# Performance work log

Hardware: AMD Instinct MI355X
Metric: run time of the kernel (lower is better)

The kernel has to match this reference:

```python
import jax, jax.numpy as jnp
import numpy as np

N = 100000
E = 1600000
IN_DIM = 128
HID = 64
NCOMM = 32


def setup_inputs() -> dict:
    key = jax.random.key(0)
    k = jax.random.split(key, 8)
    x = jax.random.normal(k[0], (N, IN_DIM), dtype=jnp.float32)
    edge_index = jax.random.randint(k[1], (2, E), 0, N, dtype=jnp.int64)
    s1 = 1.0 / np.sqrt(IN_DIM)
    s2 = 1.0 / np.sqrt(HID)
    W1 = jax.random.uniform(k[2], (IN_DIM, HID), jnp.float32, -s1, s1)
    b1 = jnp.zeros((HID,), jnp.float32)
    W2 = jax.random.uniform(k[3], (HID, HID), jnp.float32, -s2, s2)
    b2 = jnp.zeros((HID,), jnp.float32)
    Wfc = jax.random.uniform(k[4], (HID, NCOMM), jnp.float32, -s2, s2)
    bfc = jax.random.uniform(k[5], (NCOMM,), jnp.float32, -s2, s2)
    return {"x": x, "edge_index": edge_index, "W1": W1, "b1": b1,
            "W2": W2, "b2": b2, "Wfc": Wfc, "bfc": bfc}


def gcn_conv(x, row, col, norm, W, b):
    # PyG GCNConv: linear -> gather(source) * norm -> scatter_add(target) -> + bias
    h = x @ W                                    # [N, out]
    msgs = h[row] * norm[:, None]                # [E+N, out] gather (memory-bound)
    agg = jax.ops.segment_sum(msgs, col, num_segments=x.shape[0])
    return agg + b


def reference(x, edge_index, W1, b1, W2, b2, Wfc, bfc):
    n = x.shape[0]
    # add self-loops (PyG GCNConv default)
    loop = jnp.arange(n, dtype=edge_index.dtype)
    row = jnp.concatenate([edge_index[0], loop])  # source
    col = jnp.concatenate([edge_index[1], loop])  # target
    # symmetric normalization D^{-1/2} (A+I) D^{-1/2}
    deg = jax.ops.segment_sum(jnp.ones_like(col, dtype=x.dtype), col, num_segments=n)
    dinv = jnp.where(deg > 0, jax.lax.rsqrt(deg), 0.0)
    norm = dinv[row] * dinv[col]
    h = jax.nn.relu(gcn_conv(x, row, col, norm, W1, b1))   # dropout = identity (eval)
    h = jax.nn.relu(gcn_conv(h, row, col, norm, W2, b2))
    return jax.nn.sigmoid(h @ Wfc + bfc)
```

## Files before the change

kernel.cpp:

```cpp
#include <hip/hip_runtime.h>
#include <hip/hip_fp16.h>
#include <math.h>

#define N_NODES 100000
#define N_EDGES 1600000
#define IN_DIM  128
#define HID     64
#define NCOMM   32
#define NB        391
#define BSHIFT    8
#define EPB       4096
#define NBIN_BLK  391

typedef _Float16 f16x8 __attribute__((ext_vector_type(8)));
typedef float    f32x4 __attribute__((ext_vector_type(4)));

__global__ void k_detect(const unsigned int* __restrict__ e, int* __restrict__ flag) {
  int lane = threadIdx.x;
  unsigned v = 0;
  #pragma unroll
  for (int i = 0; i < 4; ++i) v |= e[2 * (lane * 4 + i) + 1];
  unsigned long long nz = __ballot(v != 0u);
  if (lane == 0) *flag = (nz == 0ull) ? 1 : 0;
}

__device__ __forceinline__ int load_idx(const int* e32, long long pos, int is64) {
  if (is64) return (int)(((const long long*)e32)[pos]);
  return e32[pos];
}

__global__ __launch_bounds__(256) void k_bhist(const int* __restrict__ e, int* __restrict__ bcnt,
                                               const int* __restrict__ flag) {
  __shared__ int cnt[NB];
  for (int i = threadIdx.x; i < NB; i += 256) cnt[i] = 0;
  __syncthreads();
  int is64 = *flag;
  long long base = (long long)blockIdx.x * EPB;
  #pragma unroll
  for (int j = 0; j < EPB / 256; ++j) {
    long long eid = base + j * 256 + threadIdx.x;
    if (eid < N_EDGES) {
      int c = load_idx(e, (long long)N_EDGES + eid, is64);
      atomicAdd(&cnt[c >> BSHIFT], 1);
    }
  }
  __syncthreads();
  for (int b = threadIdx.x; b < NB; b += 256)
    if (cnt[b]) atomicAdd(&bcnt[b], cnt[b]);
}

__global__ __launch_bounds__(512) void k_bscan(const int* __restrict__ bcnt, int* __restrict__ bptr,
                                               int* __restrict__ bcur) {
  __shared__ int sm[512];
  int t = threadIdx.x;
  int v = (t < NB) ? bcnt[t] : 0;
  sm[t] = v;
  __syncthreads();
  for (int off = 1; off < 512; off <<= 1) {
    int u = (t >= off) ? sm[t - off] : 0;
    __syncthreads();
    sm[t] += u;
    __syncthreads();
  }
  if (t < NB) {
    int ex = sm[t] - v;
    bptr[t] = ex;
    bcur[t] = ex;
  }
  if (t == 0) bptr[NB] = N_EDGES;
}

__global__ __launch_bounds__(256) void k_bin(const int* __restrict__ e, int* __restrict__ bcur,
                                             unsigned* __restrict__ ebuf, const int* __restrict__ flag) {
  __shared__ int cnt[NB];
  __shared__ int base[NB];
  for (int i = threadIdx.x; i < NB; i += 256) cnt[i] = 0;
  __syncthreads();
  int is64 = *flag;
  long long eb = (long long)blockIdx.x * EPB;
  int rr[EPB / 256], cc[EPB / 256], lr[EPB / 256];
  #pragma unroll
  for (int j = 0; j < EPB / 256; ++j) {
    long long eid = eb + j * 256 + threadIdx.x;
    if (eid < N_EDGES) {
      rr[j] = load_idx(e, eid, is64);
      cc[j] = load_idx(e, (long long)N_EDGES + eid, is64);
      lr[j] = atomicAdd(&cnt[cc[j] >> BSHIFT], 1);
    }
  }
  __syncthreads();
  for (int b = threadIdx.x; b < NB; b += 256)
    base[b] = cnt[b] ? atomicAdd(&bcur[b], cnt[b]) : 0;
  __syncthreads();
  #pragma unroll
  for (int j = 0; j < EPB / 256; ++j) {
    long long eid = eb + j * 256 + threadIdx.x;
    if (eid < N_EDGES) {
      int pos = base[cc[j] >> BSHIFT] + lr[j];
      ebuf[pos] = ((unsigned)(cc[j] & 255) << 17) | (unsigned)rr[j];
    }
  }
}

__global__ __launch_bounds__(256) void k_degsort(const unsigned* __restrict__ ebuf, const int* __restrict__ bptr,
                                                 float* __restrict__ dinv, int* __restrict__ ptr,
                                                 int* __restrict__ srow) {
  __shared__ int cnt[256];
  __shared__ int scn[256];
  __shared__ int cur[256];
  int t = threadIdx.x;
  int b = blockIdx.x;
  int c0 = b << BSHIFT;
  cnt[t] = 0;
  __syncthreads();
  int s = bptr[b], epos = bptr[b + 1];
  for (int i = s + t; i < epos; i += 256)
    atomicAdd(&cnt[ebuf[i] >> 17], 1);
  __syncthreads();
  int d = cnt[t];
  scn[t] = d;
  __syncthreads();
  for (int off = 1; off < 256; off <<= 1) {
    int u = (t >= off) ? scn[t - off] : 0;
    __syncthreads();
    scn[t] += u;
    __syncthreads();
  }
  int myptr = s + scn[t] - d;
  int node = c0 + t;
  if (node < N_NODES) {
    dinv[node] = rsqrtf((float)d + 1.0f);
    ptr[node] = myptr;
  }
  cur[t] = myptr;
  __syncthreads();
  for (int i = s + t; i < epos; i += 256) {
    unsigned w = ebuf[i];
    int pos = atomicAdd(&cur[w >> 17], 1);
    srow[pos] = (int)(w & 0x1FFFFu);
  }
  if (b == NB - 1 && t == 0) ptr[N_NODES] = N_EDGES;
}

template<int K, int M, bool FINAL, bool INH>
__global__ __launch_bounds__(256) void k_mfma(const void* __restrict__ X, const float* __restrict__ W,
                                              void* __restrict__ Y, const float* __restrict__ bias,
                                              const float* __restrict__ dscale) {
  constexpr int NN = M / 16;
  constexpr int KS = K / 32;
  __shared__ char smem[M * K * 2];

  const int tid = threadIdx.x;
  for (int i = tid; i < K * M / 4; i += 256) {
    int k  = i / (M / 4);
    int mf = (i % (M / 4)) * 4;
    float4 wv = *(const float4*)(W + (size_t)k * M + mf);
    float wa[4] = {wv.x, wv.y, wv.z, wv.w};
    #pragma unroll
    for (int c = 0; c < 4; ++c) {
      int m = mf + c;
      int byte_off = m * (2 * K) + ((((k >> 3) << 4)) ^ ((m & 7) << 4)) + (k & 7) * 2;
      *(_Float16*)(smem + byte_off) = (_Float16)wa[c];
    }
  }
  __syncthreads();

  const int lane = tid & 63;
  const int wv_  = tid >> 6;
  const int rowbase = blockIdx.x * 128 + wv_ * 32;
  const int lr = lane & 15;
  const int kg = lane >> 4;
  const int r0 = rowbase + lr;
  const int r1 = r0 + 16;
  const int rc0 = (r0 < N_NODES) ? r0 : (N_NODES - 1);
  const int rc1 = (r1 < N_NODES) ? r1 : (N_NODES - 1);

  f32x4 acc[2][NN] = {};

  #pragma unroll
  for (int ks = 0; ks < KS; ++ks) {
    const int k0 = ks * 32 + kg * 8;
    f16x8 a0, a1;
    if constexpr (!INH) {
      const float* xr = (const float*)X;
      float4 u0 = *(const float4*)(xr + (size_t)rc0 * K + k0);
      float4 u1 = *(const float4*)(xr + (size_t)rc0 * K + k0 + 4);
      float4 u2 = *(const float4*)(xr + (size_t)rc1 * K + k0);
      float4 u3 = *(const float4*)(xr + (size_t)rc1 * K + k0 + 4);
      a0[0] = (_Float16)u0.x; a0[1] = (_Float16)u0.y; a0[2] = (_Float16)u0.z; a0[3] = (_Float16)u0.w;
      a0[4] = (_Float16)u1.x; a0[5] = (_Float16)u1.y; a0[6] = (_Float16)u1.z; a0[7] = (_Float16)u1.w;
      a1[0] = (_Float16)u2.x; a1[1] = (_Float16)u2.y; a1[2] = (_Float16)u2.z; a1[3] = (_Float16)u2.w;
      a1[4] = (_Float16)u3.x; a1[5] = (_Float16)u3.y; a1[6] = (_Float16)u3.z; a1[7] = (_Float16)u3.w;
    } else {
      const char* xb = (const char*)X;
      a0 = *(const f16x8*)(xb + (size_t)rc0 * (2 * K) + k0 * 2);
      a1 = *(const f16x8*)(xb + (size_t)rc1 * (2 * K) + k0 * 2);
    }
    const int slot = (k0 >> 3) << 4;
    #pragma unroll
    for (int n = 0; n < NN; ++n) {
      const int col = n * 16 + lr;
      f16x8 b = *(const f16x8*)(smem + col * (2 * K) + (slot ^ ((col & 7) << 4)));
      acc[0][n] = __builtin_amdgcn_mfma_f32_16x16x32_f16(a0, b, acc[0][n], 0, 0, 0);
      acc[1][n] = __builtin_amdgcn_mfma_f32_16x16x32_f16(a1, b, acc[1][n], 0, 0, 0);
    }
  }

  #pragma unroll
  for (int m2 = 0; m2 < 2; ++m2) {
    #pragma unroll
    for (int r = 0; r < 4; ++r) {
      const int row = rowbase + m2 * 16 + kg * 4 + r;
      if (row < N_NODES) {
        float ds = FINAL ? 0.f : dscale[row];
        #pragma unroll
        for (int n = 0; n < NN; ++n) {
          const int col = n * 16 + lr;
          float v = acc[m2][n][r];
          if constexpr (FINAL) {
            v += bias[col];
            v = 1.f / (1.f + __expf(-v));
            ((float*)Y)[(size_t)row * M + col] = v;
          } else {
            ((__half*)Y)[(size_t)row * M + col] = __float2half(v * ds);
          }
        }
      }
    }
  }
}

__device__ __forceinline__ void addrow(float* acc, uint4 h) {
  __half2 p0 = *(__half2*)&h.x;
  __half2 p1 = *(__half2*)&h.y;
  __half2 p2 = *(__half2*)&h.z;
  __half2 p3 = *(__half2*)&h.w;
  float2 f0 = __half22float2(p0);
  float2 f1 = __half22float2(p1);
  float2 f2 = __half22float2(p2);
  float2 f3 = __half22float2(p3);
  acc[0] += f0.x; acc[1] += f0.y;
  acc[2] += f1.x; acc[3] += f1.y;
  acc[4] += f2.x; acc[5] += f2.y;
  acc[6] += f3.x; acc[7] += f3.y;
}

__global__ __launch_bounds__(256) void k_agg(const __half* __restrict__ H, __half* __restrict__ O,
                                             const int* __restrict__ ptr, const int* __restrict__ srow,
                                             const float* __restrict__ dinv, const float* __restrict__ bias) {
  int wid  = (blockIdx.x * 256 + threadIdx.x) >> 6;
  int lane = threadIdx.x & 63;
  if (wid >= N_NODES) return;
  const int q  = lane >> 3;
  const int fl = lane & 7;
  const char* Hb = (const char*)H;
  int s = ptr[wid], e = ptr[wid + 1];
  float acc[8] = {0.f, 0.f, 0.f, 0.f, 0.f, 0.f, 0.f, 0.f};
  for (int j = s; j < e; j += 16) {
    int i0 = j + q;
    int i1 = j + 8 + q;
    int r0 = srow[i0];
    int r1 = srow[i1];
    r0 = (i0 < e) ? r0 : N_NODES;
    r1 = (i1 < e) ? r1 : N_NODES;
    uint4 h0 = *(const uint4*)(Hb + (size_t)((unsigned)r0 * 128u + (unsigned)fl * 16u));
    uint4 h1 = *(const uint4*)(Hb + (size_t)((unsigned)r1 * 128u + (unsigned)fl * 16u));
    addrow(acc, h0);
    addrow(acc, h1);
  }
  if (q == 0) {
    uint4 hb = *(const uint4*)(Hb + (size_t)((unsigned)wid * 128u + (unsigned)fl * 16u));
    addrow(acc, hb);
  }
  #pragma unroll
  for (int m = 8; m < 64; m <<= 1) {
    #pragma unroll
    for (int i = 0; i < 8; ++i) acc[i] += __shfl_xor(acc[i], m, 64);
  }
  if (lane < 8) {
    float di = dinv[wid];
    float4 ba = ((const float4*)bias)[2 * fl + 0];
    float4 bb = ((const float4*)bias)[2 * fl + 1];
    __half2 o0 = __floats2half2_rn(fmaxf(acc[0] * di + ba.x, 0.f), fmaxf(acc[1] * di + ba.y, 0.f));
    __half2 o1 = __floats2half2_rn(fmaxf(acc[2] * di + ba.z, 0.f), fmaxf(acc[3] * di + ba.w, 0.f));
    __half2 o2 = __floats2half2_rn(fmaxf(acc[4] * di + bb.x, 0.f), fmaxf(acc[5] * di + bb.y, 0.f));
    __half2 o3 = __floats2half2_rn(fmaxf(acc[6] * di + bb.z, 0.f), fmaxf(acc[7] * di + bb.w, 0.f));
    uint4 pv;
    pv.x = *(unsigned*)&o0;
    pv.y = *(unsigned*)&o1;
    pv.z = *(unsigned*)&o2;
    pv.w = *(unsigned*)&o3;
    *(uint4*)((char*)O + (size_t)wid * (HID * 2) + fl * 16) = pv;
  }
}

extern "C" void kernel_launch(void* const* d_in, const int* in_sizes, int n_in,
                              void* d_out, int out_size, void* d_ws, size_t ws_size,
                              hipStream_t stream) {
  const float* x   = (const float*)d_in[0];
  const int*   e   = (const int*)d_in[1];
  const float* W1  = (const float*)d_in[2];
  const float* b1  = (const float*)d_in[3];
  const float* W2  = (const float*)d_in[4];
  const float* b2  = (const float*)d_in[5];
  const float* Wfc = (const float*)d_in[6];
  const float* bfc = (const float*)d_in[7];
  float* out = (float*)d_out;

  char* ws = (char*)d_ws;
  __half*   hbuf = (__half*)  (ws);
  unsigned* ebuf = (unsigned*)(ws);
  int*      srow = (int*)     (ws + 12800256);
  __half*   abuf = (__half*)  (ws + 19200320);
  float*    dinv = (float*)   (ws + 32000320);
  int*      ptr  = (int*)     (ws + 32400320);
  int*      flag = (int*)     (ws + 32800384);
  int*      bcnt = (int*)     (ws + 32800448);
  int*      bptr = (int*)     (ws + 32802048);
  int*      bcur = (int*)     (ws + 32803712);

  hipMemsetAsync(bcnt, 0, NB * sizeof(int), stream);
  hipMemsetAsync(ws + (size_t)N_NODES * 128, 0, 128, stream);
  k_detect<<<1, 64, 0, stream>>>((const unsigned int*)e, flag);
  k_bhist<<<NBIN_BLK, 256, 0, stream>>>(e, bcnt, flag);
  k_bscan<<<1, 512, 0, stream>>>(bcnt, bptr, bcur);
  k_bin<<<NBIN_BLK, 256, 0, stream>>>(e, bcur, ebuf, flag);
  k_degsort<<<NB, 256, 0, stream>>>(ebuf, bptr, dinv, ptr, srow);

  const int gBlocks = (N_NODES + 127) / 128;
  k_mfma<IN_DIM, HID, false, false><<<gBlocks, 256, 0, stream>>>(x, W1, hbuf, nullptr, dinv);
  k_agg<<<N_NODES * 64 / 256, 256, 0, stream>>>(hbuf, abuf, ptr, srow, dinv, b1);
  k_mfma<HID, HID, false, true><<<gBlocks, 256, 0, stream>>>(abuf, W2, hbuf, nullptr, dinv);
  k_agg<<<N_NODES * 64 / 256, 256, 0, stream>>>(hbuf, abuf, ptr, srow, dinv, b2);
  k_mfma<HID, NCOMM, true, true><<<gBlocks, 256, 0, stream>>>(abuf, Wfc, out, bfc, nullptr);
}
```

Baseline: 203.8 us.

## Use fixed-capacity bins to drop histogram/scan passes and reshape aggregation

New measurement: 219.8 us. +7.9%, slower.

```diff
diff --git a/kernel.cpp b/kernel.cpp
--- a/kernel.cpp
+++ b/kernel.cpp
@@ -9,6 +9,7 @@
 #define NCOMM   32
 #define NB        391
 #define BSHIFT    8
+#define BCAP      6144
 #define EPB       4096
 #define NBIN_BLK  391
 
@@ -29,48 +30,7 @@
   return e32[pos];
 }
 
-__global__ __launch_bounds__(256) void k_bhist(const int* __restrict__ e, int* __restrict__ bcnt,
-                                               const int* __restrict__ flag) {
-  __shared__ int cnt[NB];
-  for (int i = threadIdx.x; i < NB; i += 256) cnt[i] = 0;
-  __syncthreads();
-  int is64 = *flag;
-  long long base = (long long)blockIdx.x * EPB;
-  #pragma unroll
-  for (int j = 0; j < EPB / 256; ++j) {
-    long long eid = base + j * 256 + threadIdx.x;
-    if (eid < N_EDGES) {
-      int c = load_idx(e, (long long)N_EDGES + eid, is64);
-      atomicAdd(&cnt[c >> BSHIFT], 1);
-    }
-  }
-  __syncthreads();
-  for (int b = threadIdx.x; b < NB; b += 256)
-    if (cnt[b]) atomicAdd(&bcnt[b], cnt[b]);
-}
-
-__global__ __launch_bounds__(512) void k_bscan(const int* __restrict__ bcnt, int* __restrict__ bptr,
-                                               int* __restrict__ bcur) {
-  __shared__ int sm[512];
-  int t = threadIdx.x;
-  int v = (t < NB) ? bcnt[t] : 0;
-  sm[t] = v;
-  __syncthreads();
-  for (int off = 1; off < 512; off <<= 1) {
-    int u = (t >= off) ? sm[t - off] : 0;
-    __syncthreads();
-    sm[t] += u;
-    __syncthreads();
-  }
-  if (t < NB) {
-    int ex = sm[t] - v;
-    bptr[t] = ex;
-    bcur[t] = ex;
-  }
-  if (t == 0) bptr[NB] = N_EDGES;
-}
-
-__global__ __launch_bounds__(256) void k_bin(const int* __restrict__ e, int* __restrict__ bcur,
+__global__ __launch_bounds__(256) void k_bin(const int* __restrict__ e, int* __restrict__ bcnt,
                                              unsigned* __restrict__ ebuf, const int* __restrict__ flag) {
   __shared__ int cnt[NB];
   __shared__ int base[NB];
@@ -90,32 +50,37 @@
   }
   __syncthreads();
   for (int b = threadIdx.x; b < NB; b += 256)
-    base[b] = cnt[b] ? atomicAdd(&bcur[b], cnt[b]) : 0;
+    base[b] = cnt[b] ? atomicAdd(&bcnt[b], cnt[b]) : 0;
   __syncthreads();
   #pragma unroll
   for (int j = 0; j < EPB / 256; ++j) {
     long long eid = eb + j * 256 + threadIdx.x;
     if (eid < N_EDGES) {
-      int pos = base[cc[j] >> BSHIFT] + lr[j];
+      int bb = cc[j] >> BSHIFT;
+      int pos = bb * BCAP + base[bb] + lr[j];
       ebuf[pos] = ((unsigned)(cc[j] & 255) << 17) | (unsigned)rr[j];
     }
   }
 }
 
-__global__ __launch_bounds__(256) void k_degsort(const unsigned* __restrict__ ebuf, const int* __restrict__ bptr,
-                                                 float* __restrict__ dinv, int* __restrict__ ptr,
+__global__ __launch_bounds__(256) void k_degsort(const unsigned* __restrict__ ebuf, const int* __restrict__ bcnt,
+                                                 float* __restrict__ dinv, int2* __restrict__ parr,
                                                  int* __restrict__ srow) {
   __shared__ int cnt[256];
   __shared__ int scn[256];
   __shared__ int cur[256];
+  __shared__ unsigned eds[BCAP];
   int t = threadIdx.x;
   int b = blockIdx.x;
   int c0 = b << BSHIFT;
+  int n = bcnt[b];
   cnt[t] = 0;
   __syncthreads();
-  int s = bptr[b], epos = bptr[b + 1];
-  for (int i = s + t; i < epos; i += 256)
-    atomicAdd(&cnt[ebuf[i] >> 17], 1);
+  for (int i = t; i < n; i += 256) {
+    unsigned w = ebuf[b * BCAP + i];
+    eds[i] = w;
+    atomicAdd(&cnt[w >> 17], 1);
+  }
   __syncthreads();
   int d = cnt[t];
   scn[t] = d;
@@ -126,20 +91,19 @@
     scn[t] += u;
     __syncthreads();
   }
-  int myptr = s + scn[t] - d;
+  int sabs = b * BCAP + scn[t] - d;
   int node = c0 + t;
   if (node < N_NODES) {
     dinv[node] = rsqrtf((float)d + 1.0f);
-    ptr[node] = myptr;
-  }
-  cur[t] = myptr;
-  __syncthreads();
-  for (int i = s + t; i < epos; i += 256) {
-    unsigned w = ebuf[i];
+    parr[node] = make_int2(sabs, sabs + d);
+  }
+  cur[t] = sabs;
+  __syncthreads();
+  for (int i = t; i < n; i += 256) {
+    unsigned w = eds[i];
     int pos = atomicAdd(&cur[w >> 17], 1);
     srow[pos] = (int)(w & 0x1FFFFu);
   }
-  if (b == NB - 1 && t == 0) ptr[N_NODES] = N_EDGES;
 }
 
 template<int K, int M, bool FINAL, bool INH>
@@ -230,67 +194,36 @@
   }
 }
 
-__device__ __forceinline__ void addrow(float* acc, uint4 h) {
-  __half2 p0 = *(__half2*)&h.x;
-  __half2 p1 = *(__half2*)&h.y;
-  __half2 p2 = *(__half2*)&h.z;
-  __half2 p3 = *(__half2*)&h.w;
-  float2 f0 = __half22float2(p0);
-  float2 f1 = __half22float2(p1);
-  float2 f2 = __half22float2(p2);
-  float2 f3 = __half22float2(p3);
-  acc[0] += f0.x; acc[1] += f0.y;
-  acc[2] += f1.x; acc[3] += f1.y;
-  acc[4] += f2.x; acc[5] += f2.y;
-  acc[6] += f3.x; acc[7] += f3.y;
-}
-
 __global__ __launch_bounds__(256) void k_agg(const __half* __restrict__ H, __half* __restrict__ O,
-                                             const int* __restrict__ ptr, const int* __restrict__ srow,
+                                             const int2* __restrict__ parr, const int* __restrict__ srow,
                                              const float* __restrict__ dinv, const float* __restrict__ bias) {
   int wid  = (blockIdx.x * 256 + threadIdx.x) >> 6;
   int lane = threadIdx.x & 63;
   if (wid >= N_NODES) return;
-  const int q  = lane >> 3;
-  const int fl = lane & 7;
+  const int hf = lane >> 5;
+  const int fl = lane & 31;
   const char* Hb = (const char*)H;
-  int s = ptr[wid], e = ptr[wid + 1];
-  float acc[8] = {0.f, 0.f, 0.f, 0.f, 0.f, 0.f, 0.f, 0.f};
-  for (int j = s; j < e; j += 16) {
-    int i0 = j + q;
-    int i1 = j + 8 + q;
-    int r0 = srow[i0];
-    int r1 = srow[i1];
-    r0 = (i0 < e) ? r0 : N_NODES;
-    r1 = (i1 < e) ? r1 : N_NODES;
-    uint4 h0 = *(const uint4*)(Hb + (size_t)((unsigned)r0 * 128u + (unsigned)fl * 16u));
-    uint4 h1 = *(const uint4*)(Hb + (size_t)((unsigned)r1 * 128u + (unsigned)fl * 16u));
-    addrow(acc, h0);
-    addrow(acc, h1);
-  }
-  if (q == 0) {
-    uint4 hb = *(const uint4*)(Hb + (size_t)((unsigned)wid * 128u + (unsigned)fl * 16u));
-    addrow(acc, hb);
-  }
-  #pragma unroll
-  for (int m = 8; m < 64; m <<= 1) {
-    #pragma unroll
-    for (int i = 0; i < 8; ++i) acc[i] += __shfl_xor(acc[i], m, 64);
-  }
-  if (lane < 8) {
+  int2 se = parr[wid];
+  float ax = 0.f, ay = 0.f;
+  #pragma unroll 2
+  for (int j = se.x + hf; j < se.y; j += 2) {
+    int r = srow[j];
+    unsigned h = *(const unsigned*)(Hb + (size_t)r * 128 + fl * 4);
+    float2 f = __half22float2(*(__half2*)&h);
+    ax += f.x; ay += f.y;
+  }
+  if (hf == 0) {
+    unsigned h = *(const unsigned*)(Hb + (size_t)wid * 128 + fl * 4);
+    float2 f = __half22float2(*(__half2*)&h);
+    ax += f.x; ay += f.y;
+  }
+  ax += __shfl_xor(ax, 32, 64);
+  ay += __shfl_xor(ay, 32, 64);
+  if (lane < 32) {
     float di = dinv[wid];
-    float4 ba = ((const float4*)bias)[2 * fl + 0];
-    float4 bb = ((const float4*)bias)[2 * fl + 1];
-    __half2 o0 = __floats2half2_rn(fmaxf(acc[0] * di + ba.x, 0.f), fmaxf(acc[1] * di + ba.y, 0.f));
-    __half2 o1 = __floats2half2_rn(fmaxf(acc[2] * di + ba.z, 0.f), fmaxf(acc[3] * di + ba.w, 0.f));
-    __half2 o2 = __floats2half2_rn(fmaxf(acc[4] * di + bb.x, 0.f), fmaxf(acc[5] * di + bb.y, 0.f));
-    __half2 o3 = __floats2half2_rn(fmaxf(acc[6] * di + bb.z, 0.f), fmaxf(acc[7] * di + bb.w, 0.f));
-    uint4 pv;
-    pv.x = *(unsigned*)&o0;
-    pv.y = *(unsigned*)&o1;
-    pv.z = *(unsigned*)&o2;
-    pv.w = *(unsigned*)&o3;
-    *(uint4*)((char*)O + (size_t)wid * (HID * 2) + fl * 16) = pv;
+    float2 bv = ((const float2*)bias)[fl];
+    __half2 o = __floats2half2_rn(fmaxf(ax * di + bv.x, 0.f), fmaxf(ay * di + bv.y, 0.f));
+    *(__half2*)((char*)O + (size_t)wid * 128 + fl * 4) = o;
   }
 }
 
@@ -310,27 +243,23 @@
   char* ws = (char*)d_ws;
   __half*   hbuf = (__half*)  (ws);
   unsigned* ebuf = (unsigned*)(ws);
-  int*      srow = (int*)     (ws + 12800256);
-  __half*   abuf = (__half*)  (ws + 19200320);
-  float*    dinv = (float*)   (ws + 32000320);
-  int*      ptr  = (int*)     (ws + 32400320);
-  int*      flag = (int*)     (ws + 32800384);
-  int*      bcnt = (int*)     (ws + 32800448);
-  int*      bptr = (int*)     (ws + 32802048);
-  int*      bcur = (int*)     (ws + 32803712);
+  int*      srow = (int*)     (ws + 12800192);
+  __half*   abuf = (__half*)  (ws + 22409472);
+  float*    dinv = (float*)   (ws + 35209472);
+  int2*     parr = (int2*)    (ws + 35609472);
+  int*      flag = (int*)     (ws + 36409472);
+  int*      bcnt = (int*)     (ws + 36409536);
 
   hipMemsetAsync(bcnt, 0, NB * sizeof(int), stream);
   hipMemsetAsync(ws + (size_t)N_NODES * 128, 0, 128, stream);
   k_detect<<<1, 64, 0, stream>>>((const unsigned int*)e, flag);
-  k_bhist<<<NBIN_BLK, 256, 0, stream>>>(e, bcnt, flag);
-  k_bscan<<<1, 512, 0, stream>>>(bcnt, bptr, bcur);
-  k_bin<<<NBIN_BLK, 256, 0, stream>>>(e, bcur, ebuf, flag);
-  k_degsort<<<NB, 256, 0, stream>>>(ebuf, bptr, dinv, ptr, srow);
+  k_bin<<<NBIN_BLK, 256, 0, stream>>>(e, bcnt, ebuf, flag);
+  k_degsort<<<NB, 256, 0, stream>>>(ebuf, bcnt, dinv, parr, srow);
 
   const int gBlocks = (N_NODES + 127) / 128;
   k_mfma<IN_DIM, HID, false, false><<<gBlocks, 256, 0, stream>>>(x, W1, hbuf, nullptr, dinv);
-  k_agg<<<N_NODES * 64 / 256, 256, 0, stream>>>(hbuf, abuf, ptr, srow, dinv, b1);
+  k_agg<<<N_NODES * 64 / 256, 256, 0, stream>>>(hbuf, abuf, parr, srow, dinv, b1);
   k_mfma<HID, HID, false, true><<<gBlocks, 256, 0, stream>>>(abuf, W2, hbuf, nullptr, dinv);
-  k_agg<<<N_NODES * 64 / 256, 256, 0, stream>>>(hbuf, abuf, ptr, srow, dinv, b2);
+  k_agg<<<N_NODES * 64 / 256, 256, 0, stream>>>(hbuf, abuf, parr, srow, dinv, b2);
   k_mfma<HID, NCOMM, true, true><<<gBlocks, 256, 0, stream>>>(abuf, Wfc, out, bfc, nullptr);
 }
```
